# Kernel tuning notes

Hardware: AMD Instinct MI355X
Metric: run time of the kernel (lower is better)

## Reference

```python
import jax, jax.numpy as jnp
import numpy as np

N_NODES = 50000
N_EDGES = 400000
NODE_DIM = 128
EDGE_DIM = 64
HIDDEN = 128  # must equal NODE_DIM (index_add into zeros_like(node_feat))
EPS = 1e-8


def _param(key, shape):
    fan_in = shape[0]
    return (jax.random.normal(key, shape, jnp.float32) / np.sqrt(fan_in)).astype(jnp.float32)


def setup_inputs() -> dict:
    key = jax.random.key(0)
    ks = jax.random.split(key, 20)
    inp = {
        'node_feat': jax.random.normal(ks[0], (N_NODES, NODE_DIM), jnp.float32),
        'edge_attr': jax.random.normal(ks[1], (N_EDGES, EDGE_DIM), jnp.float32),
        'coords': 5.0 * jax.random.normal(ks[2], (N_NODES, 3), jnp.float32),
        'edge_index': jax.random.randint(ks[3], (2, N_EDGES), 0, N_NODES, dtype=jnp.int32),
        # edge_mlp: Linear(2*node+edge -> hidden), SiLU, Linear(hidden -> hidden), SiLU
        'We1': _param(ks[4], (2 * NODE_DIM + EDGE_DIM, HIDDEN)),
        'be1': jnp.zeros((HIDDEN,), jnp.float32),
        'We2': _param(ks[5], (HIDDEN, HIDDEN)),
        'be2': jnp.zeros((HIDDEN,), jnp.float32),
        # node_mlp: Linear(node+hidden -> hidden), SiLU, Linear(hidden -> node)
        'Wn1': _param(ks[6], (NODE_DIM + HIDDEN, HIDDEN)),
        'bn1': jnp.zeros((HIDDEN,), jnp.float32),
        'Wn2': _param(ks[7], (HIDDEN, NODE_DIM)),
        'bn2': jnp.zeros((NODE_DIM,), jnp.float32),
        # coord_mlp: Linear(hidden -> hidden//2), SiLU, Linear(hidden//2 -> 1)
        'Wc1': _param(ks[8], (HIDDEN, HIDDEN // 2)),
        'bc1': jnp.zeros((HIDDEN // 2,), jnp.float32),
        'Wc2': _param(ks[9], (HIDDEN // 2, 1)),
        'bc2': jnp.zeros((1,), jnp.float32),
    }
    return inp


def reference(node_feat, edge_attr, coords, edge_index,
              We1, be1, We2, be2,
              Wn1, bn1, Wn2, bn2,
              Wc1, bc1, Wc2, bc2):
    src, dst = edge_index[0], edge_index[1]
    n_nodes = node_feat.shape[0]

    # gather -> edge MLP
    edge_feat = jnp.concatenate([node_feat[src], node_feat[dst], edge_attr], axis=-1)  # [E, 2*ND+ED]
    edge_message = jax.nn.silu(jax.nn.silu(edge_feat @ We1 + be1) @ We2 + be2)         # [E, H]

    # scatter-add messages to destination nodes
    aggr = jax.ops.segment_sum(edge_message, dst, num_segments=n_nodes)                # [N, H]

    # node update (residual)
    node_in = jnp.concatenate([node_feat, aggr], axis=-1)
    node_update = jax.nn.silu(node_in @ Wn1 + bn1) @ Wn2 + bn2
    updated_nodes = node_feat + node_update

    # equivariant coordinate update
    coord_w = jax.nn.silu(edge_message @ Wc1 + bc1) @ Wc2 + bc2                        # [E, 1]
    coord_diff = coords[src] - coords[dst]                                             # [E, 3]
    coord_diff = coord_diff / (jnp.linalg.norm(coord_diff, axis=-1, keepdims=True) + EPS)
    coord_update = jax.ops.segment_sum(coord_w * coord_diff, dst, num_segments=n_nodes)
    updated_coords = coords + coord_update

    return (updated_nodes, updated_coords)
```

## Files before the change

### kernel.cpp

```cpp
#include <hip/hip_runtime.h>
#include <hip/hip_bf16.h>
#include <math.h>

#define NN 50000
#define NE 400000

typedef __attribute__((ext_vector_type(8))) short short8;
typedef __attribute__((ext_vector_type(4))) float f32x4;

#define OFF_WE1T 0
#define OFF_WE2T 40960
#define OFF_WN1T 57344
#define OFF_WN2T 90112
#define OFF_WC1T 106496
#define W_TOTAL  114688

__device__ __forceinline__ float silu_f(float x) {
    return x * (1.0f / (1.0f + __expf(-x)));
}
__device__ __forceinline__ short f2bf(float f) {
    __hip_bfloat16 b = __float2bfloat16(f);
    return *reinterpret_cast<short*>(&b);
}
__device__ __forceinline__ short8 cvt8(float4 a, float4 b) {
    short8 r;
    r[0] = f2bf(a.x); r[1] = f2bf(a.y); r[2] = f2bf(a.z); r[3] = f2bf(a.w);
    r[4] = f2bf(b.x); r[5] = f2bf(b.y); r[6] = f2bf(b.z); r[7] = f2bf(b.w);
    return r;
}

__global__ void zero_kernel(float4* __restrict__ p, int n4) {
    int i = blockIdx.x * blockDim.x + threadIdx.x;
    int st = gridDim.x * blockDim.x;
    for (; i < n4; i += st) p[i] = make_float4(0.f, 0.f, 0.f, 0.f);
}

__global__ __launch_bounds__(256) void prep_kernel(
    const float* __restrict__ We1, const float* __restrict__ We2,
    const float* __restrict__ Wn1, const float* __restrict__ Wn2,
    const float* __restrict__ Wc1, short* __restrict__ wb)
{
    const int i = blockIdx.x * 256 + threadIdx.x;
    const float* src; int N, n, k, rel;
    if (i < OFF_WE2T)      { rel = i;            src = We1; N = 128; n = rel / 320; k = rel % 320; }
    else if (i < OFF_WN1T) { rel = i - OFF_WE2T; src = We2; N = 128; n = rel / 128; k = rel % 128; }
    else if (i < OFF_WN2T) { rel = i - OFF_WN1T; src = Wn1; N = 128; n = rel / 256; k = rel % 256; }
    else if (i < OFF_WC1T) { rel = i - OFF_WN2T; src = Wn2; N = 128; n = rel / 128; k = rel % 128; }
    else                   { rel = i - OFF_WC1T; src = Wc1; N = 64;  n = rel / 128; k = rel % 128; }
    wb[i] = f2bf(src[(size_t)k * N + n]);
}

__global__ __launch_bounds__(256, 4) void edge_kernel(
    const float* __restrict__ nf, const float* __restrict__ ea,
    const float* __restrict__ coords, const int* __restrict__ ei,
    const short* __restrict__ wb,
    const float* __restrict__ be1, const float* __restrict__ be2,
    const float* __restrict__ bc1, const float* __restrict__ bc2,
    const float* __restrict__ Wc2f,
    float* __restrict__ aggr, float* __restrict__ coord_acc)
{
    __shared__ int   sS[128], sD[128];
    __shared__ short Hs[128][136];

    const int tid   = threadIdx.x;
    const int wv    = tid >> 6;
    const int lane  = tid & 63;
    const int le    = lane & 15;
    const int grp   = lane >> 4;
    const int eb    = blockIdx.x * 128;
    const int wbase = wv * 32;

    if (lane < 32) sS[wbase + lane] = ei[eb + wbase + lane];
    else           sD[wbase + (lane - 32)] = ei[NE + eb + wbase + (lane - 32)];

    const int srm0 = sS[wbase + le],      srm1 = sS[wbase + 16 + le];
    const int drm0 = sD[wbase + le],      drm1 = sD[wbase + 16 + le];

    f32x4 acc[2][8];
    #pragma unroll
    for (int m = 0; m < 2; ++m)
        #pragma unroll
        for (int t = 0; t < 8; ++t) acc[m][t] = (f32x4){0.f, 0.f, 0.f, 0.f};

    const short* w1 = wb + OFF_WE1T;
    #pragma unroll
    for (int kc = 0; kc < 10; ++kc) {
        const int gk = kc * 32 + grp * 8;
        short8 a0, a1;
        {
            const float *p0, *p1;
            if (kc < 4)      { p0 = nf + (size_t)srm0 * 128 + gk;       p1 = nf + (size_t)srm1 * 128 + gk; }
            else if (kc < 8) { p0 = nf + (size_t)drm0 * 128 + gk - 128; p1 = nf + (size_t)drm1 * 128 + gk - 128; }
            else             { p0 = ea + (size_t)(eb + wbase + le) * 64 + gk - 256;
                               p1 = ea + (size_t)(eb + wbase + 16 + le) * 64 + gk - 256; }
            a0 = cvt8(*(const float4*)p0, *(const float4*)(p0 + 4));
            a1 = cvt8(*(const float4*)p1, *(const float4*)(p1 + 4));
        }
        #pragma unroll
        for (int th = 0; th < 2; ++th) {
            short8 bf[4];
            #pragma unroll
            for (int t4 = 0; t4 < 4; ++t4)
                bf[t4] = *(const short8*)(w1 + (size_t)((th * 4 + t4) * 16 + le) * 320 + gk);
            #pragma unroll
            for (int t4 = 0; t4 < 4; ++t4) {
                acc[0][th*4+t4] = __builtin_amdgcn_mfma_f32_16x16x32_bf16(a0, bf[t4], acc[0][th*4+t4], 0, 0, 0);
                acc[1][th*4+t4] = __builtin_amdgcn_mfma_f32_16x16x32_bf16(a1, bf[t4], acc[1][th*4+t4], 0, 0, 0);
            }
        }
    }
    #pragma unroll
    for (int t = 0; t < 8; ++t) {
        const float b1 = be1[t * 16 + le];
        #pragma unroll
        for (int m = 0; m < 2; ++m)
            #pragma unroll
            for (int r = 0; r < 4; ++r)
                Hs[wbase + m * 16 + grp * 4 + r][t * 16 + le] = f2bf(silu_f(acc[m][t][r] + b1));
    }

    f32x4 acc2[2][8];
    #pragma unroll
    for (int m = 0; m < 2; ++m)
        #pragma unroll
        for (int t = 0; t < 8; ++t) acc2[m][t] = (f32x4){0.f, 0.f, 0.f, 0.f};

    const short* w2 = wb + OFF_WE2T;
    #pragma unroll
    for (int kc = 0; kc < 4; ++kc) {
        const int gk = kc * 32 + grp * 8;
        const short8 a0 = *(const short8*)&Hs[wbase + le][gk];
        const short8 a1 = *(const short8*)&Hs[wbase + 16 + le][gk];
        #pragma unroll
        for (int th = 0; th < 2; ++th) {
            short8 bf[4];
            #pragma unroll
            for (int t4 = 0; t4 < 4; ++t4)
                bf[t4] = *(const short8*)(w2 + (size_t)((th * 4 + t4) * 16 + le) * 128 + gk);
            #pragma unroll
            for (int t4 = 0; t4 < 4; ++t4) {
                acc2[0][th*4+t4] = __builtin_amdgcn_mfma_f32_16x16x32_bf16(a0, bf[t4], acc2[0][th*4+t4], 0, 0, 0);
                acc2[1][th*4+t4] = __builtin_amdgcn_mfma_f32_16x16x32_bf16(a1, bf[t4], acc2[1][th*4+t4], 0, 0, 0);
            }
        }
    }

    int dstv[2][4];
    #pragma unroll
    for (int m = 0; m < 2; ++m)
        #pragma unroll
        for (int r = 0; r < 4; ++r)
            dstv[m][r] = sD[wbase + m * 16 + grp * 4 + r];

    #pragma unroll
    for (int t = 0; t < 8; ++t) {
        const float b2 = be2[t * 16 + le];
        #pragma unroll
        for (int m = 0; m < 2; ++m)
            #pragma unroll
            for (int r = 0; r < 4; ++r) {
                const float v = silu_f(acc2[m][t][r] + b2);
                atomicAdd(&aggr[(size_t)dstv[m][r] * 128 + t * 16 + le], v);
                Hs[wbase + m * 16 + grp * 4 + r][t * 16 + le] = f2bf(v);
            }
    }

    f32x4 acc3[2][4];
    #pragma unroll
    for (int m = 0; m < 2; ++m)
        #pragma unroll
        for (int t = 0; t < 4; ++t) acc3[m][t] = (f32x4){0.f, 0.f, 0.f, 0.f};

    const short* wc = wb + OFF_WC1T;
    #pragma unroll
    for (int kc = 0; kc < 4; ++kc) {
        const int gk = kc * 32 + grp * 8;
        const short8 a0 = *(const short8*)&Hs[wbase + le][gk];
        const short8 a1 = *(const short8*)&Hs[wbase + 16 + le][gk];
        short8 bf[4];
        #pragma unroll
        for (int t4 = 0; t4 < 4; ++t4)
            bf[t4] = *(const short8*)(wc + (size_t)(t4 * 16 + le) * 128 + gk);
        #pragma unroll
        for (int t4 = 0; t4 < 4; ++t4) {
            acc3[0][t4] = __builtin_amdgcn_mfma_f32_16x16x32_bf16(a0, bf[t4], acc3[0][t4], 0, 0, 0);
            acc3[1][t4] = __builtin_amdgcn_mfma_f32_16x16x32_bf16(a1, bf[t4], acc3[1][t4], 0, 0, 0);
        }
    }

    float part[2][4];
    #pragma unroll
    for (int m = 0; m < 2; ++m)
        #pragma unroll
        for (int r = 0; r < 4; ++r) part[m][r] = 0.f;
    #pragma unroll
    for (int t = 0; t < 4; ++t) {
        const float bc = bc1[t * 16 + le];
        const float w2c = Wc2f[t * 16 + le];
        #pragma unroll
        for (int m = 0; m < 2; ++m)
            #pragma unroll
            for (int r = 0; r < 4; ++r)
                part[m][r] += silu_f(acc3[m][t][r] + bc) * w2c;
    }
    #pragma unroll
    for (int mask = 1; mask <= 8; mask <<= 1)
        #pragma unroll
        for (int m = 0; m < 2; ++m)
            #pragma unroll
            for (int r = 0; r < 4; ++r)
                part[m][r] += __shfl_xor(part[m][r], mask);

    if (le < 8) {
        const int m = le >> 2, r = le & 3;
        float v;
        if (m == 0) v = (r == 0) ? part[0][0] : (r == 1) ? part[0][1] : (r == 2) ? part[0][2] : part[0][3];
        else        v = (r == 0) ? part[1][0] : (r == 1) ? part[1][1] : (r == 2) ? part[1][2] : part[1][3];
        const int eloc = wbase + m * 16 + grp * 4 + r;
        const int s = sS[eloc], d = sD[eloc];
        const float dx = coords[3 * s + 0] - coords[3 * d + 0];
        const float dy = coords[3 * s + 1] - coords[3 * d + 1];
        const float dz = coords[3 * s + 2] - coords[3 * d + 2];
        const float wq = v + bc2[0];
        const float inv = wq / (sqrtf(dx * dx + dy * dy + dz * dz) + 1e-8f);
        atomicAdd(&coord_acc[3 * d + 0], dx * inv);
        atomicAdd(&coord_acc[3 * d + 1], dy * inv);
        atomicAdd(&coord_acc[3 * d + 2], dz * inv);
    }
}

__global__ __launch_bounds__(256, 4) void node_kernel(
    const float* __restrict__ nf, const float* __restrict__ coords,
    const short* __restrict__ wb,
    const float* __restrict__ bn1, const float* __restrict__ bn2,
    const float* __restrict__ aggr, const float* __restrict__ coord_acc,
    float* __restrict__ out)
{
    __shared__ short Hs[128][136];

    const int tid   = threadIdx.x;
    const int wv    = tid >> 6;
    const int lane  = tid & 63;
    const int le    = lane & 15;
    const int grp   = lane >> 4;
    const int nb    = blockIdx.x * 128;
    const int wbase = wv * 32;

    const int row0 = min(nb + wbase + le, NN - 1);
    const int row1 = min(nb + wbase + 16 + le, NN - 1);

    f32x4 acc[2][8];
    #pragma unroll
    for (int m = 0; m < 2; ++m)
        #pragma unroll
        for (int t = 0; t < 8; ++t) acc[m][t] = (f32x4){0.f, 0.f, 0.f, 0.f};

    const short* w1 = wb + OFF_WN1T;
    #pragma unroll
    for (int kc = 0; kc < 8; ++kc) {
        const int gk = kc * 32 + grp * 8;
        const float* p0 = (kc < 4) ? nf + (size_t)row0 * 128 + gk : aggr + (size_t)row0 * 128 + gk - 128;
        const float* p1 = (kc < 4) ? nf + (size_t)row1 * 128 + gk : aggr + (size_t)row1 * 128 + gk - 128;
        const short8 a0 = cvt8(*(const float4*)p0, *(const float4*)(p0 + 4));
        const short8 a1 = cvt8(*(const float4*)p1, *(const float4*)(p1 + 4));
        #pragma unroll
        for (int th = 0; th < 2; ++th) {
            short8 bf[4];
            #pragma unroll
            for (int t4 = 0; t4 < 4; ++t4)
                bf[t4] = *(const short8*)(w1 + (size_t)((th * 4 + t4) * 16 + le) * 256 + gk);
            #pragma unroll
            for (int t4 = 0; t4 < 4; ++t4) {
                acc[0][th*4+t4] = __builtin_amdgcn_mfma_f32_16x16x32_bf16(a0, bf[t4], acc[0][th*4+t4], 0, 0, 0);
                acc[1][th*4+t4] = __builtin_amdgcn_mfma_f32_16x16x32_bf16(a1, bf[t4], acc[1][th*4+t4], 0, 0, 0);
            }
        }
    }
    #pragma unroll
    for (int t = 0; t < 8; ++t) {
        const float b1 = bn1[t * 16 + le];
        #pragma unroll
        for (int m = 0; m < 2; ++m)
            #pragma unroll
            for (int r = 0; r < 4; ++r)
                Hs[wbase + m * 16 + grp * 4 + r][t * 16 + le] = f2bf(silu_f(acc[m][t][r] + b1));
    }

    f32x4 acc2[2][8];
    #pragma unroll
    for (int m = 0; m < 2; ++m)
        #pragma unroll
        for (int t = 0; t < 8; ++t) acc2[m][t] = (f32x4){0.f, 0.f, 0.f, 0.f};

    const short* w2 = wb + OFF_WN2T;
    #pragma unroll
    for (int kc = 0; kc < 4; ++kc) {
        const int gk = kc * 32 + grp * 8;
        const short8 a0 = *(const short8*)&Hs[wbase + le][gk];
        const short8 a1 = *(const short8*)&Hs[wbase + 16 + le][gk];
        #pragma unroll
        for (int th = 0; th < 2; ++th) {
            short8 bf[4];
            #pragma unroll
            for (int t4 = 0; t4 < 4; ++t4)
                bf[t4] = *(const short8*)(w2 + (size_t)((th * 4 + t4) * 16 + le) * 128 + gk);
            #pragma unroll
            for (int t4 = 0; t4 < 4; ++t4) {
                acc2[0][th*4+t4] = __builtin_amdgcn_mfma_f32_16x16x32_bf16(a0, bf[t4], acc2[0][th*4+t4], 0, 0, 0);
                acc2[1][th*4+t4] = __builtin_amdgcn_mfma_f32_16x16x32_bf16(a1, bf[t4], acc2[1][th*4+t4], 0, 0, 0);
            }
        }
    }
    #pragma unroll
    for (int t = 0; t < 8; ++t) {
        const float b2 = bn2[t * 16 + le];
        #pragma unroll
        for (int m = 0; m < 2; ++m)
            #pragma unroll
            for (int r = 0; r < 4; ++r) {
                const int row = nb + wbase + m * 16 + grp * 4 + r;
                if (row < NN) {
                    const int c = t * 16 + le;
                    out[(size_t)row * 128 + c] = acc2[m][t][r] + b2 + nf[(size_t)row * 128 + c];
                }
            }
    }

    for (int i = tid; i < 384; i += 256) {
        const int n = nb + i / 3, j = i % 3;
        if (n < NN)
            out[(size_t)NN * 128 + 3 * n + j] = coords[3 * n + j] + coord_acc[3 * n + j];
    }
}

extern "C" void kernel_launch(void* const* d_in, const int* in_sizes, int n_in,
                              void* d_out, int out_size, void* d_ws, size_t ws_size,
                              hipStream_t stream)
{
    const float* node_feat  = (const float*)d_in[0];
    const float* edge_attr  = (const float*)d_in[1];
    const float* coords     = (const float*)d_in[2];
    const int*   edge_index = (const int*)d_in[3];
    const float* We1 = (const float*)d_in[4];
    const float* be1 = (const float*)d_in[5];
    const float* We2 = (const float*)d_in[6];
    const float* be2 = (const float*)d_in[7];
    const float* Wn1 = (const float*)d_in[8];
    const float* bn1 = (const float*)d_in[9];
    const float* Wn2 = (const float*)d_in[10];
    const float* bn2 = (const float*)d_in[11];
    const float* Wc1 = (const float*)d_in[12];
    const float* bc1 = (const float*)d_in[13];
    const float* Wc2 = (const float*)d_in[14];
    const float* bc2 = (const float*)d_in[15];

    float* out       = (float*)d_out;
    float* aggr      = (float*)d_ws;
    float* coord_acc = aggr + (size_t)NN * 128;
    short* wbf       = (short*)(coord_acc + (size_t)NN * 3);

    prep_kernel<<<W_TOTAL / 256, 256, 0, stream>>>(We1, We2, Wn1, Wn2, Wc1, wbf);

    const int n4 = (NN * 128 + NN * 3) / 4;
    zero_kernel<<<2048, 256, 0, stream>>>((float4*)d_ws, n4);

    edge_kernel<<<NE / 128, 256, 0, stream>>>(
        node_feat, edge_attr, coords, edge_index, wbf,
        be1, be2, bc1, bc2, Wc2, aggr, coord_acc);

    node_kernel<<<(NN + 127) / 128, 256, 0, stream>>>(
        node_feat, coords, wbf, bn1, bn2, aggr, coord_acc, out);
}
```

Measured before the change: 442.5 us.

## Persistent edge kernel with LDS-resident weights, bf16 node copy, register handoff

Changes the edge kernel into a persistent kernel of 256 blocks with 768 threads. Each block stages all edge-MLP and coord-MLP weights into shared memory once, then loops over 32-edge tiles per wave. Node features are pre-converted to a bf16 copy so the gathers move half the bytes. The MFMA operands are swapped so layer outputs stay in registers and are passed to the next layer with lane shuffles instead of a shared-memory round trip. The risks are much larger LDS use per block, fewer concurrent blocks, an extra conversion pass over node features, and a fallback path when the workspace is too small.

```diff
diff --git a/kernel.cpp b/kernel.cpp
--- a/kernel.cpp
+++ b/kernel.cpp
@@ -1,6 +1,7 @@
 #include <hip/hip_runtime.h>
 #include <hip/hip_bf16.h>
 #include <math.h>
+#include <stdint.h>
 
 #define NN 50000
 #define NE 400000
@@ -22,11 +23,30 @@
     __hip_bfloat16 b = __float2bfloat16(f);
     return *reinterpret_cast<short*>(&b);
 }
+__device__ __forceinline__ uint32_t pk2(float lo, float hi) {
+    return (uint32_t)(uint16_t)f2bf(lo) | ((uint32_t)(uint16_t)f2bf(hi) << 16);
+}
 __device__ __forceinline__ short8 cvt8(float4 a, float4 b) {
     short8 r;
     r[0] = f2bf(a.x); r[1] = f2bf(a.y); r[2] = f2bf(a.z); r[3] = f2bf(a.w);
     r[4] = f2bf(b.x); r[5] = f2bf(b.y); r[6] = f2bf(b.z); r[7] = f2bf(b.w);
     return r;
+}
+
+__device__ __forceinline__ short8 exch8(uint32_t e0, uint32_t e1,
+                                        uint32_t o0, uint32_t o1,
+                                        int g, int le) {
+    const int srcA = le + 16 * ((g & 1) * 2);
+    const int srcB = srcA + 16;
+    const uint32_t a0e = __shfl((int)e0, srcA), a0o = __shfl((int)o0, srcA);
+    const uint32_t a1e = __shfl((int)e1, srcA), a1o = __shfl((int)o1, srcA);
+    const uint32_t b0e = __shfl((int)e0, srcB), b0o = __shfl((int)o0, srcB);
+    const uint32_t b1e = __shfl((int)e1, srcB), b1o = __shfl((int)o1, srcB);
+    const bool hi = (g & 2) != 0;
+    uint32_t v[4];
+    v[0] = hi ? a0o : a0e;  v[1] = hi ? a1o : a1e;
+    v[2] = hi ? b0o : b0e;  v[3] = hi ? b1o : b1e;
+    short8 r; __builtin_memcpy(&r, v, 16); return r;
 }
 
 __global__ void zero_kernel(float4* __restrict__ p, int n4) {
@@ -50,8 +70,23 @@
     wb[i] = f2bf(src[(size_t)k * N + n]);
 }
 
-__global__ __launch_bounds__(256, 4) void edge_kernel(
-    const float* __restrict__ nf, const float* __restrict__ ea,
+__global__ __launch_bounds__(256) void nf2bf_kernel(
+    const float* __restrict__ nf, short* __restrict__ nfb)
+{
+    const int n8 = NN * 128 / 8;
+    int i = blockIdx.x * blockDim.x + threadIdx.x;
+    const int st = gridDim.x * blockDim.x;
+    for (; i < n8; i += st) {
+        const float4 a = *(const float4*)&nf[(size_t)i * 8];
+        const float4 b = *(const float4*)&nf[(size_t)i * 8 + 4];
+        *(short8*)&nfb[(size_t)i * 8] = cvt8(a, b);
+    }
+}
+
+template<bool BF16NF>
+__global__ __launch_bounds__(768, 3) void edge_kernel(
+    const float* __restrict__ nf, const short* __restrict__ nfb,
+    const float* __restrict__ ea,
     const float* __restrict__ coords, const int* __restrict__ ei,
     const short* __restrict__ wb,
     const float* __restrict__ be1, const float* __restrict__ be2,
@@ -59,173 +94,166 @@
     const float* __restrict__ Wc2f,
     float* __restrict__ aggr, float* __restrict__ coord_acc)
 {
-    __shared__ int   sS[128], sD[128];
-    __shared__ short Hs[128][136];
-
-    const int tid   = threadIdx.x;
-    const int wv    = tid >> 6;
-    const int lane  = tid & 63;
-    const int le    = lane & 15;
-    const int grp   = lane >> 4;
-    const int eb    = blockIdx.x * 128;
-    const int wbase = wv * 32;
-
-    if (lane < 32) sS[wbase + lane] = ei[eb + wbase + lane];
-    else           sD[wbase + (lane - 32)] = ei[NE + eb + wbase + (lane - 32)];
-
-    const int srm0 = sS[wbase + le],      srm1 = sS[wbase + 16 + le];
-    const int drm0 = sD[wbase + le],      drm1 = sD[wbase + 16 + le];
-
-    f32x4 acc[2][8];
-    #pragma unroll
-    for (int m = 0; m < 2; ++m)
-        #pragma unroll
-        for (int t = 0; t < 8; ++t) acc[m][t] = (f32x4){0.f, 0.f, 0.f, 0.f};
-
-    const short* w1 = wb + OFF_WE1T;
-    #pragma unroll
-    for (int kc = 0; kc < 10; ++kc) {
-        const int gk = kc * 32 + grp * 8;
-        short8 a0, a1;
-        {
-            const float *p0, *p1;
-            if (kc < 4)      { p0 = nf + (size_t)srm0 * 128 + gk;       p1 = nf + (size_t)srm1 * 128 + gk; }
-            else if (kc < 8) { p0 = nf + (size_t)drm0 * 128 + gk - 128; p1 = nf + (size_t)drm1 * 128 + gk - 128; }
-            else             { p0 = ea + (size_t)(eb + wbase + le) * 64 + gk - 256;
-                               p1 = ea + (size_t)(eb + wbase + 16 + le) * 64 + gk - 256; }
-            a0 = cvt8(*(const float4*)p0, *(const float4*)(p0 + 4));
-            a1 = cvt8(*(const float4*)p1, *(const float4*)(p1 + 4));
-        }
-        #pragma unroll
-        for (int th = 0; th < 2; ++th) {
-            short8 bf[4];
-            #pragma unroll
-            for (int t4 = 0; t4 < 4; ++t4)
-                bf[t4] = *(const short8*)(w1 + (size_t)((th * 4 + t4) * 16 + le) * 320 + gk);
-            #pragma unroll
-            for (int t4 = 0; t4 < 4; ++t4) {
-                acc[0][th*4+t4] = __builtin_amdgcn_mfma_f32_16x16x32_bf16(a0, bf[t4], acc[0][th*4+t4], 0, 0, 0);
-                acc[1][th*4+t4] = __builtin_amdgcn_mfma_f32_16x16x32_bf16(a1, bf[t4], acc[1][th*4+t4], 0, 0, 0);
-            }
-        }
-    }
-    #pragma unroll
-    for (int t = 0; t < 8; ++t) {
-        const float b1 = be1[t * 16 + le];
+    __shared__ __align__(16) short W1s[128 * 328];
+    __shared__ __align__(16) short W2s[128 * 136];
+    __shared__ __align__(16) short Wcs[64 * 136];
+
+    const int tid = threadIdx.x;
+    for (int i = tid; i < 5120; i += 768) {
+        const int n = i / 40, k = (i % 40) * 8;
+        *(short8*)&W1s[n * 328 + k] = *(const short8*)&wb[OFF_WE1T + n * 320 + k];
+    }
+    for (int i = tid; i < 2048; i += 768) {
+        const int n = i >> 4, k = (i & 15) * 8;
+        *(short8*)&W2s[n * 136 + k] = *(const short8*)&wb[OFF_WE2T + n * 128 + k];
+    }
+    for (int i = tid; i < 1024; i += 768) {
+        const int n = i >> 4, k = (i & 15) * 8;
+        *(short8*)&Wcs[n * 136 + k] = *(const short8*)&wb[OFF_WC1T + n * 128 + k];
+    }
+    __syncthreads();
+
+    const int wv = tid >> 6, lane = tid & 63, le = lane & 15, g = lane >> 4;
+
+    for (int tile = blockIdx.x * 12 + wv; tile < NE / 32; tile += 256 * 12) {
+        const int base = tile * 32;
+        const int s0 = ei[base + le],      s1 = ei[base + 16 + le];
+        const int d0 = ei[NE + base + le], d1 = ei[NE + base + 16 + le];
+
+        f32x4 acc[2][8];
         #pragma unroll
         for (int m = 0; m < 2; ++m)
             #pragma unroll
-            for (int r = 0; r < 4; ++r)
-                Hs[wbase + m * 16 + grp * 4 + r][t * 16 + le] = f2bf(silu_f(acc[m][t][r] + b1));
-    }
-
-    f32x4 acc2[2][8];
-    #pragma unroll
-    for (int m = 0; m < 2; ++m)
-        #pragma unroll
-        for (int t = 0; t < 8; ++t) acc2[m][t] = (f32x4){0.f, 0.f, 0.f, 0.f};
-
-    const short* w2 = wb + OFF_WE2T;
-    #pragma unroll
-    for (int kc = 0; kc < 4; ++kc) {
-        const int gk = kc * 32 + grp * 8;
-        const short8 a0 = *(const short8*)&Hs[wbase + le][gk];
-        const short8 a1 = *(const short8*)&Hs[wbase + 16 + le][gk];
-        #pragma unroll
-        for (int th = 0; th < 2; ++th) {
-            short8 bf[4];
-            #pragma unroll
-            for (int t4 = 0; t4 < 4; ++t4)
-                bf[t4] = *(const short8*)(w2 + (size_t)((th * 4 + t4) * 16 + le) * 128 + gk);
-            #pragma unroll
-            for (int t4 = 0; t4 < 4; ++t4) {
-                acc2[0][th*4+t4] = __builtin_amdgcn_mfma_f32_16x16x32_bf16(a0, bf[t4], acc2[0][th*4+t4], 0, 0, 0);
-                acc2[1][th*4+t4] = __builtin_amdgcn_mfma_f32_16x16x32_bf16(a1, bf[t4], acc2[1][th*4+t4], 0, 0, 0);
-            }
-        }
-    }
-
-    int dstv[2][4];
-    #pragma unroll
-    for (int m = 0; m < 2; ++m)
-        #pragma unroll
-        for (int r = 0; r < 4; ++r)
-            dstv[m][r] = sD[wbase + m * 16 + grp * 4 + r];
-
-    #pragma unroll
-    for (int t = 0; t < 8; ++t) {
-        const float b2 = be2[t * 16 + le];
+            for (int t = 0; t < 8; ++t) acc[m][t] = (f32x4){0.f, 0.f, 0.f, 0.f};
+
+        #pragma unroll
+        for (int kc = 0; kc < 10; ++kc) {
+            const int gk = kc * 32 + g * 8;
+            short8 a0, a1;
+            if (kc < 8) {
+                const int r0 = (kc < 4) ? s0 : d0;
+                const int r1 = (kc < 4) ? s1 : d1;
+                const int off = gk & 127;
+                if (BF16NF) {
+                    a0 = *(const short8*)&nfb[(size_t)r0 * 128 + off];
+                    a1 = *(const short8*)&nfb[(size_t)r1 * 128 + off];
+                } else {
+                    const float* p0 = nf + (size_t)r0 * 128 + off;
+                    const float* p1 = nf + (size_t)r1 * 128 + off;
+                    a0 = cvt8(*(const float4*)p0, *(const float4*)(p0 + 4));
+                    a1 = cvt8(*(const float4*)p1, *(const float4*)(p1 + 4));
+                }
+            } else {
+                const float* p0 = ea + (size_t)(base + le) * 64 + gk - 256;
+                const float* p1 = ea + (size_t)(base + 16 + le) * 64 + gk - 256;
+                a0 = cvt8(*(const float4*)p0, *(const float4*)(p0 + 4));
+                a1 = cvt8(*(const float4*)p1, *(const float4*)(p1 + 4));
+            }
+            #pragma unroll
+            for (int t = 0; t < 8; ++t) {
+                const short8 wf = *(const short8*)&W1s[(t * 16 + le) * 328 + gk];
+                acc[0][t] = __builtin_amdgcn_mfma_f32_16x16x32_bf16(wf, a0, acc[0][t], 0, 0, 0);
+                acc[1][t] = __builtin_amdgcn_mfma_f32_16x16x32_bf16(wf, a1, acc[1][t], 0, 0, 0);
+            }
+        }
+
+        uint32_t hp[2][8][2];
+        #pragma unroll
+        for (int t = 0; t < 8; ++t) {
+            const float4 b = *(const float4*)&be1[t * 16 + g * 4];
+            #pragma unroll
+            for (int m = 0; m < 2; ++m) {
+                const float x0 = silu_f(acc[m][t][0] + b.x);
+                const float x1 = silu_f(acc[m][t][1] + b.y);
+                const float x2 = silu_f(acc[m][t][2] + b.z);
+                const float x3 = silu_f(acc[m][t][3] + b.w);
+                hp[m][t][0] = pk2(x0, x1);
+                hp[m][t][1] = pk2(x2, x3);
+            }
+        }
+
+        f32x4 acc2[2][8];
         #pragma unroll
         for (int m = 0; m < 2; ++m)
             #pragma unroll
-            for (int r = 0; r < 4; ++r) {
-                const float v = silu_f(acc2[m][t][r] + b2);
-                atomicAdd(&aggr[(size_t)dstv[m][r] * 128 + t * 16 + le], v);
-                Hs[wbase + m * 16 + grp * 4 + r][t * 16 + le] = f2bf(v);
-            }
-    }
-
-    f32x4 acc3[2][4];
-    #pragma unroll
-    for (int m = 0; m < 2; ++m)
-        #pragma unroll
-        for (int t = 0; t < 4; ++t) acc3[m][t] = (f32x4){0.f, 0.f, 0.f, 0.f};
-
-    const short* wc = wb + OFF_WC1T;
-    #pragma unroll
-    for (int kc = 0; kc < 4; ++kc) {
-        const int gk = kc * 32 + grp * 8;
-        const short8 a0 = *(const short8*)&Hs[wbase + le][gk];
-        const short8 a1 = *(const short8*)&Hs[wbase + 16 + le][gk];
-        short8 bf[4];
-        #pragma unroll
-        for (int t4 = 0; t4 < 4; ++t4)
-            bf[t4] = *(const short8*)(wc + (size_t)(t4 * 16 + le) * 128 + gk);
-        #pragma unroll
-        for (int t4 = 0; t4 < 4; ++t4) {
-            acc3[0][t4] = __builtin_amdgcn_mfma_f32_16x16x32_bf16(a0, bf[t4], acc3[0][t4], 0, 0, 0);
-            acc3[1][t4] = __builtin_amdgcn_mfma_f32_16x16x32_bf16(a1, bf[t4], acc3[1][t4], 0, 0, 0);
-        }
-    }
-
-    float part[2][4];
-    #pragma unroll
-    for (int m = 0; m < 2; ++m)
-        #pragma unroll
-        for (int r = 0; r < 4; ++r) part[m][r] = 0.f;
-    #pragma unroll
-    for (int t = 0; t < 4; ++t) {
-        const float bc = bc1[t * 16 + le];
-        const float w2c = Wc2f[t * 16 + le];
+            for (int t = 0; t < 8; ++t) acc2[m][t] = (f32x4){0.f, 0.f, 0.f, 0.f};
+
+        #pragma unroll
+        for (int cc = 0; cc < 4; ++cc) {
+            const int gk = cc * 32 + g * 8;
+            const short8 x0 = exch8(hp[0][cc*2][0], hp[0][cc*2][1], hp[0][cc*2+1][0], hp[0][cc*2+1][1], g, le);
+            const short8 x1 = exch8(hp[1][cc*2][0], hp[1][cc*2][1], hp[1][cc*2+1][0], hp[1][cc*2+1][1], g, le);
+            #pragma unroll
+            for (int t = 0; t < 8; ++t) {
+                const short8 wf = *(const short8*)&W2s[(t * 16 + le) * 136 + gk];
+                acc2[0][t] = __builtin_amdgcn_mfma_f32_16x16x32_bf16(wf, x0, acc2[0][t], 0, 0, 0);
+                acc2[1][t] = __builtin_amdgcn_mfma_f32_16x16x32_bf16(wf, x1, acc2[1][t], 0, 0, 0);
+            }
+        }
+
+        #pragma unroll
+        for (int t = 0; t < 8; ++t) {
+            const float4 b = *(const float4*)&be2[t * 16 + g * 4];
+            #pragma unroll
+            for (int m = 0; m < 2; ++m) {
+                const int dst = m ? d1 : d0;
+                float* abase = aggr + (size_t)dst * 128 + t * 16 + g * 4;
+                const float x0 = silu_f(acc2[m][t][0] + b.x);
+                const float x1 = silu_f(acc2[m][t][1] + b.y);
+                const float x2 = silu_f(acc2[m][t][2] + b.z);
+                const float x3 = silu_f(acc2[m][t][3] + b.w);
+                atomicAdd(abase + 0, x0);
+                atomicAdd(abase + 1, x1);
+                atomicAdd(abase + 2, x2);
+                atomicAdd(abase + 3, x3);
+                hp[m][t][0] = pk2(x0, x1);
+                hp[m][t][1] = pk2(x2, x3);
+            }
+        }
+
+        f32x4 acc3[2][4];
         #pragma unroll
         for (int m = 0; m < 2; ++m)
             #pragma unroll
-            for (int r = 0; r < 4; ++r)
-                part[m][r] += silu_f(acc3[m][t][r] + bc) * w2c;
-    }
-    #pragma unroll
-    for (int mask = 1; mask <= 8; mask <<= 1)
-        #pragma unroll
-        for (int m = 0; m < 2; ++m)
-            #pragma unroll
-            for (int r = 0; r < 4; ++r)
-                part[m][r] += __shfl_xor(part[m][r], mask);
-
-    if (le < 8) {
-        const int m = le >> 2, r = le & 3;
-        float v;
-        if (m == 0) v = (r == 0) ? part[0][0] : (r == 1) ? part[0][1] : (r == 2) ? part[0][2] : part[0][3];
-        else        v = (r == 0) ? part[1][0] : (r == 1) ? part[1][1] : (r == 2) ? part[1][2] : part[1][3];
-        const int eloc = wbase + m * 16 + grp * 4 + r;
-        const int s = sS[eloc], d = sD[eloc];
-        const float dx = coords[3 * s + 0] - coords[3 * d + 0];
-        const float dy = coords[3 * s + 1] - coords[3 * d + 1];
-        const float dz = coords[3 * s + 2] - coords[3 * d + 2];
-        const float wq = v + bc2[0];
-        const float inv = wq / (sqrtf(dx * dx + dy * dy + dz * dz) + 1e-8f);
-        atomicAdd(&coord_acc[3 * d + 0], dx * inv);
-        atomicAdd(&coord_acc[3 * d + 1], dy * inv);
-        atomicAdd(&coord_acc[3 * d + 2], dz * inv);
+            for (int t = 0; t < 4; ++t) acc3[m][t] = (f32x4){0.f, 0.f, 0.f, 0.f};
+
+        #pragma unroll
+        for (int cc = 0; cc < 4; ++cc) {
+            const int gk = cc * 32 + g * 8;
+            const short8 x0 = exch8(hp[0][cc*2][0], hp[0][cc*2][1], hp[0][cc*2+1][0], hp[0][cc*2+1][1], g, le);
+            const short8 x1 = exch8(hp[1][cc*2][0], hp[1][cc*2][1], hp[1][cc*2+1][0], hp[1][cc*2+1][1], g, le);
+            #pragma unroll
+            for (int t = 0; t < 4; ++t) {
+                const short8 wf = *(const short8*)&Wcs[(t * 16 + le) * 136 + gk];
+                acc3[0][t] = __builtin_amdgcn_mfma_f32_16x16x32_bf16(wf, x0, acc3[0][t], 0, 0, 0);
+                acc3[1][t] = __builtin_amdgcn_mfma_f32_16x16x32_bf16(wf, x1, acc3[1][t], 0, 0, 0);
+            }
+        }
+
+        float part0 = 0.f, part1 = 0.f;
+        #pragma unroll
+        for (int t = 0; t < 4; ++t) {
+            const float4 bc = *(const float4*)&bc1[t * 16 + g * 4];
+            const float4 wc = *(const float4*)&Wc2f[t * 16 + g * 4];
+            part0 += silu_f(acc3[0][t][0] + bc.x) * wc.x + silu_f(acc3[0][t][1] + bc.y) * wc.y
+                   + silu_f(acc3[0][t][2] + bc.z) * wc.z + silu_f(acc3[0][t][3] + bc.w) * wc.w;
+            part1 += silu_f(acc3[1][t][0] + bc.x) * wc.x + silu_f(acc3[1][t][1] + bc.y) * wc.y
+                   + silu_f(acc3[1][t][2] + bc.z) * wc.z + silu_f(acc3[1][t][3] + bc.w) * wc.w;
+        }
+        part0 += __shfl_xor(part0, 16); part0 += __shfl_xor(part0, 32);
+        part1 += __shfl_xor(part1, 16); part1 += __shfl_xor(part1, 32);
+
+        if (g < 2) {
+            const int s = g ? s1 : s0, d = g ? d1 : d0;
+            const float wq = (g ? part1 : part0) + bc2[0];
+            const float dx = coords[3 * s + 0] - coords[3 * d + 0];
+            const float dy = coords[3 * s + 1] - coords[3 * d + 1];
+            const float dz = coords[3 * s + 2] - coords[3 * d + 2];
+            const float inv = wq / (sqrtf(dx * dx + dy * dy + dz * dz) + 1e-8f);
+            atomicAdd(&coord_acc[3 * d + 0], dx * inv);
+            atomicAdd(&coord_acc[3 * d + 1], dy * inv);
+            atomicAdd(&coord_acc[3 * d + 2], dz * inv);
+        }
     }
 }
 
@@ -358,15 +386,27 @@
     float* aggr      = (float*)d_ws;
     float* coord_acc = aggr + (size_t)NN * 128;
     short* wbf       = (short*)(coord_acc + (size_t)NN * 3);
+    short* nfb       = wbf + W_TOTAL;
+
+    const size_t need = ((size_t)NN * 128 + (size_t)NN * 3) * 4
+                      + ((size_t)W_TOTAL + (size_t)NN * 128) * 2;
+    const bool use_bf = ws_size >= need;
 
     prep_kernel<<<W_TOTAL / 256, 256, 0, stream>>>(We1, We2, Wn1, Wn2, Wc1, wbf);
+    if (use_bf)
+        nf2bf_kernel<<<2048, 256, 0, stream>>>(node_feat, nfb);
 
     const int n4 = (NN * 128 + NN * 3) / 4;
     zero_kernel<<<2048, 256, 0, stream>>>((float4*)d_ws, n4);
 
-    edge_kernel<<<NE / 128, 256, 0, stream>>>(
-        node_feat, edge_attr, coords, edge_index, wbf,
-        be1, be2, bc1, bc2, Wc2, aggr, coord_acc);
+    if (use_bf)
+        edge_kernel<true><<<256, 768, 0, stream>>>(
+            node_feat, nfb, edge_attr, coords, edge_index, wbf,
+            be1, be2, bc1, bc2, Wc2, aggr, coord_acc);
+    else
+        edge_kernel<false><<<256, 768, 0, stream>>>(
+            node_feat, nfb, edge_attr, coords, edge_index, wbf,
+            be1, be2, bc1, bc2, Wc2, aggr, coord_acc);
 
     node_kernel<<<(NN + 127) / 128, 256, 0, stream>>>(
         node_feat, coords, wbf, bn1, bn2, aggr, coord_acc, out);
```

After: 867.4 us. 1.96x slower.

## Pre-convert node and edge features to bf16 and stage gathers via LDS loads

Applied to the files above, without the earlier changes.

A widened prep kernel converts node features and edge attributes to bf16 buffers in workspace. The edge kernel then gathers half-width bf16 rows straight into per-wave LDS with global_load_lds, issuing all gathers up front before the MFMA loop, and takes edge indices from shuffles instead of shared arrays. The goal is to cut the gather bytes and conversion work in the hot edge kernel and to overlap gather latency. The cost is an extra full pass over the inputs (about 100 MB read plus 58 MB written), lower occupancy from launch_bounds 2 and 16 KB of LDS per wave, and a fallback path when the workspace is too small.

```diff
diff --git a/kernel.cpp b/kernel.cpp
--- a/kernel.cpp
+++ b/kernel.cpp
@@ -1,6 +1,7 @@
 #include <hip/hip_runtime.h>
 #include <hip/hip_bf16.h>
 #include <math.h>
+#include <stdint.h>
 
 #define NN 50000
 #define NE 400000
@@ -15,6 +16,9 @@
 #define OFF_WC1T 106496
 #define W_TOTAL  114688
 
+#define NFB_ITEMS 800000
+#define EAB_ITEMS 3200000
+
 __device__ __forceinline__ float silu_f(float x) {
     return x * (1.0f / (1.0f + __expf(-x)));
 }
@@ -29,6 +33,12 @@
     return r;
 }
 
+__device__ __forceinline__ void gload16(const short* g, short* l) {
+    __builtin_amdgcn_global_load_lds(
+        (const __attribute__((address_space(1))) void*)g,
+        (__attribute__((address_space(3))) void*)l, 16, 0, 0);
+}
+
 __global__ void zero_kernel(float4* __restrict__ p, int n4) {
     int i = blockIdx.x * blockDim.x + threadIdx.x;
     int st = gridDim.x * blockDim.x;
@@ -38,20 +48,37 @@
 __global__ __launch_bounds__(256) void prep_kernel(
     const float* __restrict__ We1, const float* __restrict__ We2,
     const float* __restrict__ Wn1, const float* __restrict__ Wn2,
-    const float* __restrict__ Wc1, short* __restrict__ wb)
+    const float* __restrict__ Wc1, const float* __restrict__ nf,
+    const float* __restrict__ ea,
+    short* __restrict__ wb, short* __restrict__ nfb, short* __restrict__ eab,
+    int full)
 {
     const int i = blockIdx.x * 256 + threadIdx.x;
-    const float* src; int N, n, k, rel;
-    if (i < OFF_WE2T)      { rel = i;            src = We1; N = 128; n = rel / 320; k = rel % 320; }
-    else if (i < OFF_WN1T) { rel = i - OFF_WE2T; src = We2; N = 128; n = rel / 128; k = rel % 128; }
-    else if (i < OFF_WN2T) { rel = i - OFF_WN1T; src = Wn1; N = 128; n = rel / 256; k = rel % 256; }
-    else if (i < OFF_WC1T) { rel = i - OFF_WN2T; src = Wn2; N = 128; n = rel / 128; k = rel % 128; }
-    else                   { rel = i - OFF_WC1T; src = Wc1; N = 64;  n = rel / 128; k = rel % 128; }
-    wb[i] = f2bf(src[(size_t)k * N + n]);
-}
-
-__global__ __launch_bounds__(256, 4) void edge_kernel(
-    const float* __restrict__ nf, const float* __restrict__ ea,
+    if (i < W_TOTAL) {
+        const float* src; int N, n, k, rel;
+        if (i < OFF_WE2T)      { rel = i;            src = We1; N = 128; n = rel / 320; k = rel % 320; }
+        else if (i < OFF_WN1T) { rel = i - OFF_WE2T; src = We2; N = 128; n = rel / 128; k = rel % 128; }
+        else if (i < OFF_WN2T) { rel = i - OFF_WN1T; src = Wn1; N = 128; n = rel / 256; k = rel % 256; }
+        else if (i < OFF_WC1T) { rel = i - OFF_WN2T; src = Wn2; N = 128; n = rel / 128; k = rel % 128; }
+        else                   { rel = i - OFF_WC1T; src = Wc1; N = 64;  n = rel / 128; k = rel % 128; }
+        wb[i] = f2bf(src[(size_t)k * N + n]);
+    } else if (full && i < W_TOTAL + NFB_ITEMS) {
+        const int j = i - W_TOTAL;
+        const float4 a = *(const float4*)&nf[(size_t)j * 8];
+        const float4 b = *(const float4*)&nf[(size_t)j * 8 + 4];
+        *(short8*)&nfb[(size_t)j * 8] = cvt8(a, b);
+    } else if (full && i < W_TOTAL + NFB_ITEMS + EAB_ITEMS) {
+        const int j = i - W_TOTAL - NFB_ITEMS;
+        const float4 a = *(const float4*)&ea[(size_t)j * 8];
+        const float4 b = *(const float4*)&ea[(size_t)j * 8 + 4];
+        *(short8*)&eab[(size_t)j * 8] = cvt8(a, b);
+    }
+}
+
+template<bool STAGED>
+__global__ __launch_bounds__(256, 2) void edge_kernel(
+    const float* __restrict__ nf, const short* __restrict__ nfb,
+    const float* __restrict__ ea, const short* __restrict__ eab,
     const float* __restrict__ coords, const int* __restrict__ ei,
     const short* __restrict__ wb,
     const float* __restrict__ be1, const float* __restrict__ be2,
@@ -59,22 +86,35 @@
     const float* __restrict__ Wc2f,
     float* __restrict__ aggr, float* __restrict__ coord_acc)
 {
-    __shared__ int   sS[128], sD[128];
-    __shared__ short Hs[128][136];
-
-    const int tid   = threadIdx.x;
-    const int wv    = tid >> 6;
-    const int lane  = tid & 63;
-    const int le    = lane & 15;
-    const int grp   = lane >> 4;
-    const int eb    = blockIdx.x * 128;
-    const int wbase = wv * 32;
-
-    if (lane < 32) sS[wbase + lane] = ei[eb + wbase + lane];
-    else           sD[wbase + (lane - 32)] = ei[NE + eb + wbase + (lane - 32)];
-
-    const int srm0 = sS[wbase + le],      srm1 = sS[wbase + 16 + le];
-    const int drm0 = sD[wbase + le],      drm1 = sD[wbase + 16 + le];
+    __shared__ short smem[4][8192];
+
+    const int tid = threadIdx.x;
+    const int wv = tid >> 6, lane = tid & 63, le = lane & 15, g = lane >> 4;
+    const int base = (blockIdx.x * 4 + wv) * 32;
+    short* stage = smem[wv];
+    short (*Hs)[136] = (short(*)[136])stage;
+
+    const int s0 = ei[base + le],      s1 = ei[base + 16 + le];
+    const int d0 = ei[NE + base + le], d1 = ei[NE + base + 16 + le];
+
+    short8 ea8[2][2];
+    if constexpr (STAGED) {
+        #pragma unroll
+        for (int kc = 0; kc < 8; ++kc) {
+            const int r0 = (kc < 4) ? s0 : d0;
+            const int r1 = (kc < 4) ? s1 : d1;
+            const int col = (kc & 3) * 32 + g * 8;
+            gload16(nfb + (size_t)r0 * 128 + col, stage + (kc * 2 + 0) * 512);
+            gload16(nfb + (size_t)r1 * 128 + col, stage + (kc * 2 + 1) * 512);
+        }
+        #pragma unroll
+        for (int q = 0; q < 2; ++q) {
+            ea8[0][q] = *(const short8*)&eab[(size_t)(base + le) * 64 + q * 32 + g * 8];
+            ea8[1][q] = *(const short8*)&eab[(size_t)(base + 16 + le) * 64 + q * 32 + g * 8];
+        }
+        asm volatile("s_waitcnt vmcnt(0)" ::: "memory");
+        __builtin_amdgcn_sched_barrier(0);
+    }
 
     f32x4 acc[2][8];
     #pragma unroll
@@ -85,30 +125,43 @@
     const short* w1 = wb + OFF_WE1T;
     #pragma unroll
     for (int kc = 0; kc < 10; ++kc) {
-        const int gk = kc * 32 + grp * 8;
+        const int gk = kc * 32 + g * 8;
         short8 a0, a1;
-        {
-            const float *p0, *p1;
-            if (kc < 4)      { p0 = nf + (size_t)srm0 * 128 + gk;       p1 = nf + (size_t)srm1 * 128 + gk; }
-            else if (kc < 8) { p0 = nf + (size_t)drm0 * 128 + gk - 128; p1 = nf + (size_t)drm1 * 128 + gk - 128; }
-            else             { p0 = ea + (size_t)(eb + wbase + le) * 64 + gk - 256;
-                               p1 = ea + (size_t)(eb + wbase + 16 + le) * 64 + gk - 256; }
-            a0 = cvt8(*(const float4*)p0, *(const float4*)(p0 + 4));
-            a1 = cvt8(*(const float4*)p1, *(const float4*)(p1 + 4));
-        }
-        #pragma unroll
-        for (int th = 0; th < 2; ++th) {
-            short8 bf[4];
-            #pragma unroll
-            for (int t4 = 0; t4 < 4; ++t4)
-                bf[t4] = *(const short8*)(w1 + (size_t)((th * 4 + t4) * 16 + le) * 320 + gk);
-            #pragma unroll
-            for (int t4 = 0; t4 < 4; ++t4) {
-                acc[0][th*4+t4] = __builtin_amdgcn_mfma_f32_16x16x32_bf16(a0, bf[t4], acc[0][th*4+t4], 0, 0, 0);
-                acc[1][th*4+t4] = __builtin_amdgcn_mfma_f32_16x16x32_bf16(a1, bf[t4], acc[1][th*4+t4], 0, 0, 0);
+        if (kc < 8) {
+            if constexpr (STAGED) {
+                a0 = *(const short8*)&stage[(kc * 2 + 0) * 512 + lane * 8];
+                a1 = *(const short8*)&stage[(kc * 2 + 1) * 512 + lane * 8];
+            } else {
+                const int r0 = (kc < 4) ? s0 : d0;
+                const int r1 = (kc < 4) ? s1 : d1;
+                const int col = (kc & 3) * 32 + g * 8;
+                const float* p0 = nf + (size_t)r0 * 128 + col;
+                const float* p1 = nf + (size_t)r1 * 128 + col;
+                a0 = cvt8(*(const float4*)p0, *(const float4*)(p0 + 4));
+                a1 = cvt8(*(const float4*)p1, *(const float4*)(p1 + 4));
             }
-        }
-    }
+        } else {
+            if constexpr (STAGED) {
+                a0 = ea8[0][kc - 8];
+                a1 = ea8[1][kc - 8];
+            } else {
+                const float* p0 = ea + (size_t)(base + le) * 64 + (kc - 8) * 32 + g * 8;
+                const float* p1 = ea + (size_t)(base + 16 + le) * 64 + (kc - 8) * 32 + g * 8;
+                a0 = cvt8(*(const float4*)p0, *(const float4*)(p0 + 4));
+                a1 = cvt8(*(const float4*)p1, *(const float4*)(p1 + 4));
+            }
+        }
+        short8 bfv[8];
+        #pragma unroll
+        for (int t = 0; t < 8; ++t)
+            bfv[t] = *(const short8*)(w1 + (size_t)(t * 16 + le) * 320 + gk);
+        #pragma unroll
+        for (int t = 0; t < 8; ++t) {
+            acc[0][t] = __builtin_amdgcn_mfma_f32_16x16x32_bf16(a0, bfv[t], acc[0][t], 0, 0, 0);
+            acc[1][t] = __builtin_amdgcn_mfma_f32_16x16x32_bf16(a1, bfv[t], acc[1][t], 0, 0, 0);
+        }
+    }
+
     #pragma unroll
     for (int t = 0; t < 8; ++t) {
         const float b1 = be1[t * 16 + le];
@@ -116,7 +169,7 @@
         for (int m = 0; m < 2; ++m)
             #pragma unroll
             for (int r = 0; r < 4; ++r)
-                Hs[wbase + m * 16 + grp * 4 + r][t * 16 + le] = f2bf(silu_f(acc[m][t][r] + b1));
+                Hs[m * 16 + g * 4 + r][t * 16 + le] = f2bf(silu_f(acc[m][t][r] + b1));
     }
 
     f32x4 acc2[2][8];
@@ -128,30 +181,26 @@
     const short* w2 = wb + OFF_WE2T;
     #pragma unroll
     for (int kc = 0; kc < 4; ++kc) {
-        const int gk = kc * 32 + grp * 8;
-        const short8 a0 = *(const short8*)&Hs[wbase + le][gk];
-        const short8 a1 = *(const short8*)&Hs[wbase + 16 + le][gk];
-        #pragma unroll
-        for (int th = 0; th < 2; ++th) {
-            short8 bf[4];
-            #pragma unroll
-            for (int t4 = 0; t4 < 4; ++t4)
-                bf[t4] = *(const short8*)(w2 + (size_t)((th * 4 + t4) * 16 + le) * 128 + gk);
-            #pragma unroll
-            for (int t4 = 0; t4 < 4; ++t4) {
-                acc2[0][th*4+t4] = __builtin_amdgcn_mfma_f32_16x16x32_bf16(a0, bf[t4], acc2[0][th*4+t4], 0, 0, 0);
-                acc2[1][th*4+t4] = __builtin_amdgcn_mfma_f32_16x16x32_bf16(a1, bf[t4], acc2[1][th*4+t4], 0, 0, 0);
-            }
+        const int gk = kc * 32 + g * 8;
+        const short8 a0 = *(const short8*)&Hs[le][gk];
+        const short8 a1 = *(const short8*)&Hs[16 + le][gk];
+        short8 bfv[8];
+        #pragma unroll
+        for (int t = 0; t < 8; ++t)
+            bfv[t] = *(const short8*)(w2 + (size_t)(t * 16 + le) * 128 + gk);
+        #pragma unroll
+        for (int t = 0; t < 8; ++t) {
+            acc2[0][t] = __builtin_amdgcn_mfma_f32_16x16x32_bf16(a0, bfv[t], acc2[0][t], 0, 0, 0);
+            acc2[1][t] = __builtin_amdgcn_mfma_f32_16x16x32_bf16(a1, bfv[t], acc2[1][t], 0, 0, 0);
         }
     }
 
     int dstv[2][4];
     #pragma unroll
-    for (int m = 0; m < 2; ++m)
-        #pragma unroll
-        for (int r = 0; r < 4; ++r)
-            dstv[m][r] = sD[wbase + m * 16 + grp * 4 + r];
-
+    for (int r = 0; r < 4; ++r) {
+        dstv[0][r] = __shfl(d0, g * 4 + r);
+        dstv[1][r] = __shfl(d1, g * 4 + r);
+    }
     #pragma unroll
     for (int t = 0; t < 8; ++t) {
         const float b2 = be2[t * 16 + le];
@@ -161,7 +210,7 @@
             for (int r = 0; r < 4; ++r) {
                 const float v = silu_f(acc2[m][t][r] + b2);
                 atomicAdd(&aggr[(size_t)dstv[m][r] * 128 + t * 16 + le], v);
-                Hs[wbase + m * 16 + grp * 4 + r][t * 16 + le] = f2bf(v);
+                Hs[m * 16 + g * 4 + r][t * 16 + le] = f2bf(v);
             }
     }
 
@@ -174,17 +223,17 @@
     const short* wc = wb + OFF_WC1T;
     #pragma unroll
     for (int kc = 0; kc < 4; ++kc) {
-        const int gk = kc * 32 + grp * 8;
-        const short8 a0 = *(const short8*)&Hs[wbase + le][gk];
-        const short8 a1 = *(const short8*)&Hs[wbase + 16 + le][gk];
-        short8 bf[4];
-        #pragma unroll
-        for (int t4 = 0; t4 < 4; ++t4)
-            bf[t4] = *(const short8*)(wc + (size_t)(t4 * 16 + le) * 128 + gk);
-        #pragma unroll
-        for (int t4 = 0; t4 < 4; ++t4) {
-            acc3[0][t4] = __builtin_amdgcn_mfma_f32_16x16x32_bf16(a0, bf[t4], acc3[0][t4], 0, 0, 0);
-            acc3[1][t4] = __builtin_amdgcn_mfma_f32_16x16x32_bf16(a1, bf[t4], acc3[1][t4], 0, 0, 0);
+        const int gk = kc * 32 + g * 8;
+        const short8 a0 = *(const short8*)&Hs[le][gk];
+        const short8 a1 = *(const short8*)&Hs[16 + le][gk];
+        short8 bfv[4];
+        #pragma unroll
+        for (int t = 0; t < 4; ++t)
+            bfv[t] = *(const short8*)(wc + (size_t)(t * 16 + le) * 128 + gk);
+        #pragma unroll
+        for (int t = 0; t < 4; ++t) {
+            acc3[0][t] = __builtin_amdgcn_mfma_f32_16x16x32_bf16(a0, bfv[t], acc3[0][t], 0, 0, 0);
+            acc3[1][t] = __builtin_amdgcn_mfma_f32_16x16x32_bf16(a1, bfv[t], acc3[1][t], 0, 0, 0);
         }
     }
 
@@ -210,14 +259,17 @@
             #pragma unroll
             for (int r = 0; r < 4; ++r)
                 part[m][r] += __shfl_xor(part[m][r], mask);
+
+    const int rr = le & 3;
+    const int sA = __shfl(s0, g * 4 + rr), sB = __shfl(s1, g * 4 + rr);
+    const int dA = __shfl(d0, g * 4 + rr), dB = __shfl(d1, g * 4 + rr);
 
     if (le < 8) {
         const int m = le >> 2, r = le & 3;
         float v;
         if (m == 0) v = (r == 0) ? part[0][0] : (r == 1) ? part[0][1] : (r == 2) ? part[0][2] : part[0][3];
         else        v = (r == 0) ? part[1][0] : (r == 1) ? part[1][1] : (r == 2) ? part[1][2] : part[1][3];
-        const int eloc = wbase + m * 16 + grp * 4 + r;
-        const int s = sS[eloc], d = sD[eloc];
+        const int s = m ? sB : sA, d = m ? dB : dA;
         const float dx = coords[3 * s + 0] - coords[3 * d + 0];
         const float dy = coords[3 * s + 1] - coords[3 * d + 1];
         const float dz = coords[3 * s + 2] - coords[3 * d + 2];
@@ -229,23 +281,19 @@
     }
 }
 
-__global__ __launch_bounds__(256, 4) void node_kernel(
-    const float* __restrict__ nf, const float* __restrict__ coords,
-    const short* __restrict__ wb,
+template<bool BF16NF>
+__global__ __launch_bounds__(256, 2) void node_kernel(
+    const float* __restrict__ nf, const short* __restrict__ nfb,
+    const float* __restrict__ coords, const short* __restrict__ wb,
     const float* __restrict__ bn1, const float* __restrict__ bn2,
     const float* __restrict__ aggr, const float* __restrict__ coord_acc,
     float* __restrict__ out)
 {
     __shared__ short Hs[128][136];
 
-    const int tid   = threadIdx.x;
-    const int wv    = tid >> 6;
-    const int lane  = tid & 63;
-    const int le    = lane & 15;
-    const int grp   = lane >> 4;
-    const int nb    = blockIdx.x * 128;
-    const int wbase = wv * 32;
-
+    const int tid = threadIdx.x;
+    const int wv = tid >> 6, lane = tid & 63, le = lane & 15, grp = lane >> 4;
+    const int nb = blockIdx.x * 128, wbase = wv * 32;
     const int row0 = min(nb + wbase + le, NN - 1);
     const int row1 = min(nb + wbase + 16 + le, NN - 1);
 
@@ -259,21 +307,31 @@
     #pragma unroll
     for (int kc = 0; kc < 8; ++kc) {
         const int gk = kc * 32 + grp * 8;
-        const float* p0 = (kc < 4) ? nf + (size_t)row0 * 128 + gk : aggr + (size_t)row0 * 128 + gk - 128;
-        const float* p1 = (kc < 4) ? nf + (size_t)row1 * 128 + gk : aggr + (size_t)row1 * 128 + gk - 128;
-        const short8 a0 = cvt8(*(const float4*)p0, *(const float4*)(p0 + 4));
-        const short8 a1 = cvt8(*(const float4*)p1, *(const float4*)(p1 + 4));
-        #pragma unroll
-        for (int th = 0; th < 2; ++th) {
-            short8 bf[4];
-            #pragma unroll
-            for (int t4 = 0; t4 < 4; ++t4)
-                bf[t4] = *(const short8*)(w1 + (size_t)((th * 4 + t4) * 16 + le) * 256 + gk);
-            #pragma unroll
-            for (int t4 = 0; t4 < 4; ++t4) {
-                acc[0][th*4+t4] = __builtin_amdgcn_mfma_f32_16x16x32_bf16(a0, bf[t4], acc[0][th*4+t4], 0, 0, 0);
-                acc[1][th*4+t4] = __builtin_amdgcn_mfma_f32_16x16x32_bf16(a1, bf[t4], acc[1][th*4+t4], 0, 0, 0);
+        short8 a0, a1;
+        if (kc < 4) {
+            if (BF16NF) {
+                a0 = *(const short8*)&nfb[(size_t)row0 * 128 + gk];
+                a1 = *(const short8*)&nfb[(size_t)row1 * 128 + gk];
+            } else {
+                const float* p0 = nf + (size_t)row0 * 128 + gk;
+                const float* p1 = nf + (size_t)row1 * 128 + gk;
+                a0 = cvt8(*(const float4*)p0, *(const float4*)(p0 + 4));
+                a1 = cvt8(*(const float4*)p1, *(const float4*)(p1 + 4));
             }
+        } else {
+            const float* p0 = aggr + (size_t)row0 * 128 + gk - 128;
+            const float* p1 = aggr + (size_t)row1 * 128 + gk - 128;
+            a0 = cvt8(*(const float4*)p0, *(const float4*)(p0 + 4));
+            a1 = cvt8(*(const float4*)p1, *(const float4*)(p1 + 4));
+        }
+        short8 bfv[8];
+        #pragma unroll
+        for (int t = 0; t < 8; ++t)
+            bfv[t] = *(const short8*)(w1 + (size_t)(t * 16 + le) * 256 + gk);
+        #pragma unroll
+        for (int t = 0; t < 8; ++t) {
+            acc[0][t] = __builtin_amdgcn_mfma_f32_16x16x32_bf16(a0, bfv[t], acc[0][t], 0, 0, 0);
+            acc[1][t] = __builtin_amdgcn_mfma_f32_16x16x32_bf16(a1, bfv[t], acc[1][t], 0, 0, 0);
         }
     }
     #pragma unroll
@@ -298,17 +356,14 @@
         const int gk = kc * 32 + grp * 8;
         const short8 a0 = *(const short8*)&Hs[wbase + le][gk];
         const short8 a1 = *(const short8*)&Hs[wbase + 16 + le][gk];
-        #pragma unroll
-        for (int th = 0; th < 2; ++th) {
-            short8 bf[4];
-            #pragma unroll
-            for (int t4 = 0; t4 < 4; ++t4)
-                bf[t4] = *(const short8*)(w2 + (size_t)((th * 4 + t4) * 16 + le) * 128 + gk);
-            #pragma unroll
-            for (int t4 = 0; t4 < 4; ++t4) {
-                acc2[0][th*4+t4] = __builtin_amdgcn_mfma_f32_16x16x32_bf16(a0, bf[t4], acc2[0][th*4+t4], 0, 0, 0);
-                acc2[1][th*4+t4] = __builtin_amdgcn_mfma_f32_16x16x32_bf16(a1, bf[t4], acc2[1][th*4+t4], 0, 0, 0);
-            }
+        short8 bfv[8];
+        #pragma unroll
+        for (int t = 0; t < 8; ++t)
+            bfv[t] = *(const short8*)(w2 + (size_t)(t * 16 + le) * 128 + gk);
+        #pragma unroll
+        for (int t = 0; t < 8; ++t) {
+            acc2[0][t] = __builtin_amdgcn_mfma_f32_16x16x32_bf16(a0, bfv[t], acc2[0][t], 0, 0, 0);
+            acc2[1][t] = __builtin_amdgcn_mfma_f32_16x16x32_bf16(a1, bfv[t], acc2[1][t], 0, 0, 0);
         }
     }
     #pragma unroll
@@ -353,21 +408,50 @@
     const float* bc1 = (const float*)d_in[13];
     const float* Wc2 = (const float*)d_in[14];
     const float* bc2 = (const float*)d_in[15];
-
-    float* out       = (float*)d_out;
-    float* aggr      = (float*)d_ws;
-    float* coord_acc = aggr + (size_t)NN * 128;
-    short* wbf       = (short*)(coord_acc + (size_t)NN * 3);
-
-    prep_kernel<<<W_TOTAL / 256, 256, 0, stream>>>(We1, We2, Wn1, Wn2, Wc1, wbf);
+    float* out = (float*)d_out;
+
+    const size_t sz_wb   = (size_t)W_TOTAL * 2;
+    const size_t sz_agg  = (size_t)NN * 128 * 4;
+    const size_t sz_cac  = (size_t)NN * 3 * 4;
+    const size_t sz_nfb  = (size_t)NN * 128 * 2;
+    const size_t sz_eab  = (size_t)NE * 64 * 2;
+    const size_t need_full = sz_wb + sz_agg + sz_cac + sz_nfb + sz_eab;
+    const size_t need_min  = sz_wb + sz_agg + sz_cac;
+
+    char* p = (char*)d_ws;
+    short* wbf       = (short*)p;  p += sz_wb;
+    float* aggr      = (float*)p;  p += sz_agg;
+    float* coord_acc = (float*)p;  p += sz_cac;
+    short* nfb       = (short*)p;  p += sz_nfb;
+    short* eab       = (short*)p;
 
     const int n4 = (NN * 128 + NN * 3) / 4;
-    zero_kernel<<<2048, 256, 0, stream>>>((float4*)d_ws, n4);
-
-    edge_kernel<<<NE / 128, 256, 0, stream>>>(
-        node_feat, edge_attr, coords, edge_index, wbf,
-        be1, be2, bc1, bc2, Wc2, aggr, coord_acc);
-
-    node_kernel<<<(NN + 127) / 128, 256, 0, stream>>>(
-        node_feat, coords, wbf, bn1, bn2, aggr, coord_acc, out);
-}
+    const int eg = NE / 128;
+    const int ng = (NN + 127) / 128;
+
+    if (ws_size >= need_full) {
+        const int pg = (W_TOTAL + NFB_ITEMS + EAB_ITEMS + 255) / 256;
+        prep_kernel<<<pg, 256, 0, stream>>>(
+            We1, We2, Wn1, Wn2, Wc1, node_feat, edge_attr, wbf, nfb, eab, 1);
+        zero_kernel<<<2048, 256, 0, stream>>>((float4*)aggr, n4);
+
+        edge_kernel<true><<<eg, 256, 0, stream>>>(
+            node_feat, nfb, edge_attr, eab, coords, edge_index, wbf,
+            be1, be2, bc1, bc2, Wc2, aggr, coord_acc);
+
+        node_kernel<true><<<ng, 256, 0, stream>>>(
+            node_feat, nfb, coords, wbf, bn1, bn2, aggr, coord_acc, out);
+    } else {
+        const int pg = (W_TOTAL + 255) / 256;
+        prep_kernel<<<pg, 256, 0, stream>>>(
+            We1, We2, Wn1, Wn2, Wc1, node_feat, edge_attr, wbf, nullptr, nullptr, 0);
+        zero_kernel<<<2048, 256, 0, stream>>>((float4*)aggr, n4);
+
+        edge_kernel<false><<<eg, 256, 0, stream>>>(
+            node_feat, nullptr, edge_attr, nullptr, coords, edge_index, wbf,
+            be1, be2, bc1, bc2, Wc2, aggr, coord_acc);
+
+        node_kernel<false><<<ng, 256, 0, stream>>>(
+            node_feat, nullptr, coords, wbf, bn1, bn2, aggr, coord_acc, out);
+    }
+}
```

After: 405.1 us. 1.09x faster.
